# Performance work log

Hardware: AMD Instinct MI355X
Metric: run time of the kernel (lower is better)

Reference implementation:

```python
import jax, jax.numpy as jnp
import numpy as np

NUM_HEADS = 16
EMBED = 1024
HEAD = EMBED // NUM_HEADS  # 64
MAX_DIST = 4
NEG_INF = -1e30


def setup_inputs() -> dict:
    key = jax.random.key(0)
    ks = jax.random.split(key, 8)
    B, S = 2, 2048
    x = jax.random.normal(ks[0], (B, S, EMBED), dtype=jnp.float32)
    return {
        "k": x,  # self-attention: k == v == q values
        "v": x,
        "q": x,
        "Wk": jax.random.normal(ks[1], (EMBED, EMBED), dtype=jnp.float32) * 0.02,
        "Wv": jax.random.normal(ks[2], (EMBED, EMBED), dtype=jnp.float32) * 0.02,
        "Wq": jax.random.normal(ks[3], (EMBED, EMBED), dtype=jnp.float32) * 0.02,
        "Wo": jax.random.normal(ks[4], (EMBED, EMBED), dtype=jnp.float32) * 0.02,
        "p_params": jax.random.normal(ks[5], (HEAD, 2 * MAX_DIST + 1), dtype=jnp.float32) * 0.02,
    }


def reference(k, v, q, Wk, Wv, Wq, Wo, p_params):
    B, Kl, _ = k.shape
    Ql = q.shape[1]
    # torch nn.Linear(bias=False): y = x @ W.T
    kh = (k @ Wk.T).reshape(B, Kl, NUM_HEADS, HEAD).transpose(0, 2, 1, 3)
    vh = (v @ Wv.T).reshape(B, Kl, NUM_HEADS, HEAD).transpose(0, 2, 1, 3)
    qh = (q @ Wq.T).reshape(B, Ql, NUM_HEADS, HEAD).transpose(0, 2, 1, 3)
    qh = qh / jnp.sqrt(jnp.float32(HEAD))
    # content scores: [B,H,Q,K]
    scores0 = jnp.einsum("bhqd,bhkd->bhqk", qh, kh)
    # relative-position bias: q . p_params[:, r] for each bucket r, then gather per (i,j)
    bias = jnp.einsum("bhqd,dr->bhqr", qh, p_params)  # [B,H,Q,2M+1]
    d = jnp.clip(jnp.arange(Ql)[:, None] - jnp.arange(Kl)[None, :], -MAX_DIST, MAX_DIST) + MAX_DIST  # [Q,K]
    rel = bias[:, :, jnp.arange(Ql)[:, None], d]  # [B,H,Q,K]
    scores = scores0 + rel
    # causal mask
    causal = jnp.arange(Ql)[:, None] >= jnp.arange(Kl)[None, :]
    scores = jnp.where(causal[None, None], scores, NEG_INF)
    attn = jax.nn.softmax(scores, axis=-1)
    out = jnp.einsum("bhqk,bhkd->bhqd", attn, vh)
    out = out.transpose(0, 2, 1, 3).reshape(B, Ql, EMBED)
    return out @ Wo.T
```

## Files before the change

kernel.cpp:

```cpp
#include <hip/hip_runtime.h>


using short8  = __attribute__((ext_vector_type(8))) short;
using floatx4 = __attribute__((ext_vector_type(4))) float;
using float4v = __attribute__((ext_vector_type(4))) float;
using ushort4v = __attribute__((ext_vector_type(4))) unsigned short;
using uint2v  = __attribute__((ext_vector_type(2))) unsigned int;

#define LOG2E 1.4426950408889634f

__device__ __forceinline__ unsigned short f2bf(float f) {
  unsigned u = __float_as_uint(f);
  return (unsigned short)((u + 0x7FFFu + ((u >> 16) & 1u)) >> 16);
}
__device__ __forceinline__ float bf2f(unsigned short s) {
  return __uint_as_float(((unsigned)s) << 16);
}
__device__ __forceinline__ unsigned cvt_pk_bf16(float lo, float hi) {
  unsigned r;
  asm("v_cvt_pk_bf16_f32 %0, %1, %2" : "=v"(r) : "v"(lo), "v"(hi));
  return r;
}
__device__ __forceinline__ void gload_lds16(const void* g, void* l) {
  __builtin_amdgcn_global_load_lds(
      (const __attribute__((address_space(1))) unsigned int*)g,
      (__attribute__((address_space(3))) unsigned int*)l, 16, 0, 0);
}

__global__ void f2bf_kern(const float* __restrict__ in,
                          unsigned short* __restrict__ out, int n4) {
  int i = blockIdx.x * 256 + threadIdx.x;
  if (i >= n4) return;
  float4v v = ((const float4v*)in)[i];
  ushort4v o;
  o[0] = f2bf(v[0]); o[1] = f2bf(v[1]); o[2] = f2bf(v[2]); o[3] = f2bf(v[3]);
  ((ushort4v*)out)[i] = o;
}

__global__ void f2bfW_kern(const float* __restrict__ w0, unsigned short* o0,
                           const float* __restrict__ w1, unsigned short* o1,
                           const float* __restrict__ w2, unsigned short* o2,
                           const float* __restrict__ w3, unsigned short* o3) {
  int i = blockIdx.x * 256 + threadIdx.x;
  const float* in;
  unsigned short* out;
  switch (blockIdx.y) {
    case 0: in = w0; out = o0; break;
    case 1: in = w1; out = o1; break;
    case 2: in = w2; out = o2; break;
    default: in = w3; out = o3; break;
  }
  float4v v = ((const float4v*)in)[i];
  ushort4v o;
  o[0] = f2bf(v[0]); o[1] = f2bf(v[1]); o[2] = f2bf(v[2]); o[3] = f2bf(v[3]);
  ((ushort4v*)out)[i] = o;
}

__device__ __forceinline__ void gemm_core(
    const unsigned short* __restrict__ A, const unsigned short* __restrict__ B,
    void* __restrict__ Cv, int N, int K, int mBase, int nBase, float alpha,
    bool outbf, unsigned short* As, unsigned short* Bs) {
  const int tid = threadIdx.x;
  const int lane = tid & 63;
  const int w = tid >> 6;
  const int wr = w >> 1, wc = w & 1;
  const int lr = lane & 15, lg = lane >> 4;

  floatx4 acc[4][4] = {};

  for (int k0 = 0; k0 < K; k0 += 32) {
#pragma unroll
    for (int i = 0; i < 2; ++i) {
      int idx = i * 256 + tid;
      int row = idx >> 2, c8 = (idx & 3) * 8;
      gload_lds16(A + (size_t)(mBase + row) * K + (k0 + c8), As + idx * 8);
      gload_lds16(B + (size_t)(nBase + row) * K + (k0 + c8), Bs + idx * 8);
    }
    __syncthreads();
    short8 af[4], bfr[4];
#pragma unroll
    for (int mf = 0; mf < 4; ++mf)
      af[mf] = *(const short8*)(As + (wr * 64 + mf * 16 + lr) * 32 + lg * 8);
#pragma unroll
    for (int nf = 0; nf < 4; ++nf)
      bfr[nf] = *(const short8*)(Bs + (wc * 64 + nf * 16 + lr) * 32 + lg * 8);
#pragma unroll
    for (int mf = 0; mf < 4; ++mf)
#pragma unroll
      for (int nf = 0; nf < 4; ++nf)
        acc[mf][nf] = __builtin_amdgcn_mfma_f32_16x16x32_bf16(
            af[mf], bfr[nf], acc[mf][nf], 0, 0, 0);
    __syncthreads();
  }

#pragma unroll
  for (int mf = 0; mf < 4; ++mf)
#pragma unroll
    for (int nf = 0; nf < 4; ++nf)
#pragma unroll
      for (int r = 0; r < 4; ++r) {
        size_t row = (size_t)mBase + wr * 64 + mf * 16 + lg * 4 + r;
        size_t col = (size_t)nBase + wc * 64 + nf * 16 + lr;
        float v = acc[mf][nf][r] * alpha;
        if (outbf)
          ((unsigned short*)Cv)[row * (size_t)N + col] = f2bf(v);
        else
          ((float*)Cv)[row * (size_t)N + col] = v;
      }
}

__global__ __launch_bounds__(256, 2) void proj3_kern(
    const unsigned short* __restrict__ xbf, const unsigned short* __restrict__ wkb,
    unsigned short* __restrict__ khb,
    const unsigned short* __restrict__ wqb, unsigned short* __restrict__ qhb,
    const unsigned short* __restrict__ wvb, unsigned short* __restrict__ vtb) {
  __shared__ alignas(16) unsigned short As[128 * 32];
  __shared__ alignas(16) unsigned short Bs[128 * 32];
  int z = blockIdx.z;
  if (z == 0)
    gemm_core(xbf, wkb, khb, 1024, 1024, blockIdx.y * 128, blockIdx.x * 128,
              1.0f, true, As, Bs);
  else if (z == 1)
    gemm_core(xbf, wqb, qhb, 1024, 1024, blockIdx.y * 128, blockIdx.x * 128,
              0.125f, true, As, Bs);
  else
    gemm_core(wvb, xbf, vtb, 4096, 1024, blockIdx.x * 128, blockIdx.y * 128,
              1.0f, true, As, Bs);
}

__global__ __launch_bounds__(256, 2) void gemm_out_kern(
    const unsigned short* __restrict__ A, const unsigned short* __restrict__ B,
    float* __restrict__ C) {
  __shared__ alignas(16) unsigned short As[128 * 32];
  __shared__ alignas(16) unsigned short Bs[128 * 32];
  gemm_core(A, B, C, 1024, 1024, blockIdx.y * 128, blockIdx.x * 128, 1.0f,
            false, As, Bs);
}

__global__ __launch_bounds__(256, 3) void attn_kern(
    const unsigned short* __restrict__ qh,
    const unsigned short* __restrict__ kh,
    const unsigned short* __restrict__ vt,
    const float* __restrict__ pp,
    unsigned short* __restrict__ ao,
    unsigned short* __restrict__ opart,
    float* __restrict__ mbuf,
    float* __restrict__ lbuf) {
  __shared__ alignas(16) char smem[44032];
  unsigned short* Qs  = (unsigned short*)smem;
  unsigned short* Vs1 = (unsigned short*)(smem + 8192);
  unsigned short* Ks0 = (unsigned short*)(smem + 16384);
  unsigned short* Vs0 = (unsigned short*)(smem + 24576);
  unsigned short* Ps  = (unsigned short*)(smem + 32768);
  float* biasS = (float*)(smem + 40960);
  float* ppS   = (float*)(smem + 32768);

  const int tid = threadIdx.x;
  const int lane = tid & 63;
  const int w = tid >> 6;
  const int lr = lane & 15, lg = lane >> 4;
  const int hb = blockIdx.x;
  const int h = hb & 15, b = hb >> 4;
  const int u = blockIdx.y;

  int qt, k0, k1;
  if (u == 0)       { qt = 15;     k0 = 0;  k1 = 16; }
  else if (u <= 16) { qt = 15 + u; k0 = 0;  k1 = 16; }
  else if (u == 17) { qt = 31;     k0 = 16; k1 = 32; }
  else {
    int p = (u - 18) >> 1;
    if (((u - 18) & 1) == 0) { qt = 14 - p; k0 = 0;  k1 = qt + 1; }
    else                     { qt = 30 - p; k0 = 16; k1 = qt + 1; }
  }
  const bool partial = (qt >= 16);
  const int qbase = qt * 64;
  const size_t bsQ = (size_t)b * 2048 + qbase;

  const unsigned short* khB = kh + ((size_t)b * 2048) * 1024 + h * 64;
  const unsigned short* vtB = vt + ((size_t)h * 64) * 4096 + b * 2048;

  auto stage_kv = [&](int kbase, unsigned short* Kd, unsigned short* Vd) {
#pragma unroll
    for (int i = 0; i < 2; ++i) {
      int idx = i * 256 + tid;
      int row = idx >> 3, pc = idx & 7;
      int cl = pc ^ (row & 7);
      gload_lds16(khB + ((size_t)(kbase + row) << 10) + cl * 8, Kd + idx * 8);
      gload_lds16(vtB + ((size_t)row << 12) + kbase + cl * 8, Vd + idx * 8);
    }
  };

#pragma unroll
  for (int i = 0; i < 2; ++i) {
    int idx = i * 256 + tid;
    int row = idx >> 3, c8 = (idx & 7) * 8;
    gload_lds16(qh + (bsQ + row) * 1024 + h * 64 + c8, Qs + idx * 8);
  }
  for (int idx = tid; idx < 576; idx += 256) {
    int r = idx >> 6, d = idx & 63;
    ppS[r * 64 + d] = pp[d * 9 + r];
  }
  stage_kv(k0 * 64, Ks0, Vs0);
  __syncthreads();

  const int qrowL = w * 16 + lr;
  short8 aq[2];
#pragma unroll
  for (int c = 0; c < 2; ++c)
    aq[c] = *(const short8*)(Qs + qrowL * 64 + c * 32 + lg * 8);

  for (int idx = tid; idx < 576; idx += 256) {
    int row = idx / 9, r = idx - row * 9;
    const unsigned short* qrow = Qs + row * 64;
    const float* pr = ppS + r * 64;
    float s = 0.f;
#pragma unroll
    for (int d8 = 0; d8 < 8; ++d8) {
      short8 qv = *(const short8*)(qrow + d8 * 8);
#pragma unroll
      for (int j = 0; j < 8; ++j)
        s += bf2f((unsigned short)qv[j]) * pr[d8 * 8 + j];
    }
    biasS[row * 12 + r] = s;
  }
  __syncthreads();

  const int q_glob = qbase + w * 16 + lr;
  const float b8 = biasS[qrowL * 12 + 8];
  unsigned short* Pw = Ps + w * 1024;

  float m_run = -1e30f, l_run = 0.f;
  floatx4 o[4] = {};

  for (int kt = k0; kt < k1; ++kt) {
    const int kbase = kt * 64;
    const int cur = (kt - k0) & 1;
    unsigned short* Kc = cur ? Qs : Ks0;
    unsigned short* Vc = cur ? Vs1 : Vs0;
    if (kt + 1 < k1)
      stage_kv(kbase + 64, cur ? Ks0 : Qs, cur ? Vs0 : Vs1);

    floatx4 sa[4] = {};
    __builtin_amdgcn_s_setprio(1);
#pragma unroll
    for (int kf = 0; kf < 4; ++kf)
#pragma unroll
      for (int c = 0; c < 2; ++c) {
        int row = kf * 16 + lr;
        short8 ak = *(const short8*)(Kc + row * 64 +
                                     (((c * 4 + lg) ^ (lr & 7)) * 8));
        sa[kf] = __builtin_amdgcn_mfma_f32_16x16x32_bf16(ak, aq[c], sa[kf],
                                                         0, 0, 0);
      }
    __builtin_amdgcn_s_setprio(0);

    float bext;
    if (qbase + w * 16 >= kbase + 67) {
      bext = b8;
    } else {
      bext = 0.f;
#pragma unroll
      for (int kf = 0; kf < 4; ++kf)
#pragma unroll
        for (int r = 0; r < 4; ++r) {
          int dq = q_glob - (kbase + kf * 16 + lg * 4 + r);
          if (dq < 0)
            sa[kf][r] = -1e30f;
          else
            sa[kf][r] += biasS[qrowL * 12 + (dq > 4 ? 8 : dq + 4)];
        }
    }

    float mx = -1e30f;
#pragma unroll
    for (int kf = 0; kf < 4; ++kf)
#pragma unroll
      for (int r = 0; r < 4; ++r) mx = fmaxf(mx, sa[kf][r]);
    mx += bext;
    mx = fmaxf(mx, __shfl_xor(mx, 16, 64));
    mx = fmaxf(mx, __shfl_xor(mx, 32, 64));
    if (__any(mx > m_run + 8.f)) {
      float mn = fmaxf(m_run, mx);
      float al = __builtin_amdgcn_exp2f((m_run - mn) * LOG2E);
      m_run = mn;
      l_run *= al;
      float alo[4];
#pragma unroll
      for (int r = 0; r < 4; ++r) alo[r] = __shfl(al, lg * 4 + r, 64);
#pragma unroll
      for (int df = 0; df < 4; ++df)
#pragma unroll
        for (int r = 0; r < 4; ++r) o[df][r] *= alo[r];
    }

    const float c1 = (bext - m_run) * LOG2E;
    float rs = 0.f;
#pragma unroll
    for (int kf = 0; kf < 4; ++kf) {
      float p0 = __builtin_amdgcn_exp2f(fmaf(sa[kf][0], LOG2E, c1));
      float p1 = __builtin_amdgcn_exp2f(fmaf(sa[kf][1], LOG2E, c1));
      float p2 = __builtin_amdgcn_exp2f(fmaf(sa[kf][2], LOG2E, c1));
      float p3 = __builtin_amdgcn_exp2f(fmaf(sa[kf][3], LOG2E, c1));
      rs += (p0 + p1) + (p2 + p3);
      uint2v pk;
      pk[0] = cvt_pk_bf16(p0, p1);
      pk[1] = cvt_pk_bf16(p2, p3);
      int phys = (kf * 2 + (lg >> 1)) ^ (lr & 7);
      *(uint2v*)(Pw + lr * 64 + phys * 8 + (lg & 1) * 4) = pk;
    }
    rs += __shfl_xor(rs, 16, 64);
    rs += __shfl_xor(rs, 32, 64);
    l_run += rs;

    __builtin_amdgcn_s_setprio(1);
#pragma unroll
    for (int c = 0; c < 2; ++c) {
      short8 pa = *(const short8*)(Pw + lr * 64 +
                                   (((c * 4 + lg) ^ (lr & 7)) * 8));
#pragma unroll
      for (int df = 0; df < 4; ++df) {
        int row = df * 16 + lr;
        short8 bv = *(const short8*)(Vc + row * 64 +
                                     (((c * 4 + lg) ^ (lr & 7)) * 8));
        o[df] = __builtin_amdgcn_mfma_f32_16x16x32_bf16(pa, bv, o[df],
                                                        0, 0, 0);
      }
    }
    __builtin_amdgcn_s_setprio(0);
    __syncthreads();
  }

  if (!partial) {
    float rl[4];
#pragma unroll
    for (int r = 0; r < 4; ++r)
      rl[r] = __builtin_amdgcn_rcpf(__shfl(l_run, lg * 4 + r, 64));
    const size_t outRow0 = bsQ + w * 16 + lg * 4;
#pragma unroll
    for (int df = 0; df < 4; ++df)
#pragma unroll
      for (int r = 0; r < 4; ++r)
        ao[(outRow0 + r) * 1024 + h * 64 + df * 16 + lr] =
            f2bf(o[df][r] * rl[r]);
  } else {
    const int pid = (hb * 16 + (qt - 16)) * 2 + (k0 == 16 ? 1 : 0);
    unsigned short* op = opart + (size_t)pid * 4096;
#pragma unroll
    for (int df = 0; df < 4; ++df)
#pragma unroll
      for (int r = 0; r < 4; ++r)
        op[(w * 16 + lg * 4 + r) * 64 + df * 16 + lr] = f2bf(o[df][r]);
    if (lg == 0) {
      mbuf[pid * 64 + w * 16 + lr] = m_run;
      lbuf[pid * 64 + w * 16 + lr] = l_run;
    }
  }
}

__global__ void combine_kern(const unsigned short* __restrict__ opart,
                             const float* __restrict__ mbuf,
                             const float* __restrict__ lbuf,
                             unsigned short* __restrict__ ao) {
  const int t = blockIdx.x;
  const int hb = t >> 4;
  const int qtl = t & 15;
  const int qt = 16 + qtl;
  const int b = hb >> 4, h = hb & 15;
  const int pid0 = (hb * 16 + qtl) * 2, pid1 = pid0 + 1;
  const int row = threadIdx.x >> 2;
  const int colg = (threadIdx.x & 3) * 16;

  float m1 = mbuf[pid0 * 64 + row], m2 = mbuf[pid1 * 64 + row];
  float l1 = lbuf[pid0 * 64 + row], l2 = lbuf[pid1 * 64 + row];
  float m = fmaxf(m1, m2);
  float s1 = __builtin_amdgcn_exp2f((m1 - m) * LOG2E);
  float s2 = __builtin_amdgcn_exp2f((m2 - m) * LOG2E);
  float linv = 1.f / fmaf(l1, s1, l2 * s2);
  s1 *= linv; s2 *= linv;

  const unsigned short* O1 = opart + (size_t)pid0 * 4096 + row * 64 + colg;
  const unsigned short* O2 = opart + (size_t)pid1 * 4096 + row * 64 + colg;
  unsigned short* dst =
      ao + ((size_t)b * 2048 + qt * 64 + row) * 1024 + h * 64 + colg;
#pragma unroll
  for (int i = 0; i < 2; ++i) {
    short8 a = *(const short8*)(O1 + i * 8);
    short8 c = *(const short8*)(O2 + i * 8);
    short8 ov;
#pragma unroll
    for (int j = 0; j < 8; ++j)
      ov[j] = (short)f2bf(fmaf(bf2f((unsigned short)a[j]), s1,
                               bf2f((unsigned short)c[j]) * s2));
    *(short8*)(dst + i * 8) = ov;
  }
}

extern "C" void kernel_launch(void* const* d_in, const int* in_sizes, int n_in,
                              void* d_out, int out_size, void* d_ws,
                              size_t ws_size, hipStream_t stream) {
  const float* k_in = (const float*)d_in[0];
  const float* Wk = (const float*)d_in[3];
  const float* Wv = (const float*)d_in[4];
  const float* Wq = (const float*)d_in[5];
  const float* Wo = (const float*)d_in[6];
  const float* pp = (const float*)d_in[7];

  const size_t NX = 4096u * 1024u;
  const size_t NW = 1024u * 1024u;
  unsigned short* ws = (unsigned short*)d_ws;
  unsigned short* xbf = ws;
  unsigned short* wkb = xbf + NX;
  unsigned short* wvb = wkb + NW;
  unsigned short* wqb = wvb + NW;
  unsigned short* wob = wqb + NW;
  unsigned short* khb = wob + NW;
  unsigned short* vtb = khb + NX;
  unsigned short* qhb = vtb + NX;
  unsigned short* aob = qhb + NX;
  unsigned short* opart = aob + NX;
  float* mbuf = (float*)(opart + NX);
  float* lbuf = mbuf + 1024 * 64;

  (void)in_sizes; (void)n_in; (void)out_size; (void)ws_size;

  f2bf_kern<<<dim3(4096), dim3(256), 0, stream>>>(k_in, xbf, (int)(NX / 4));
  f2bfW_kern<<<dim3(1024, 4), dim3(256), 0, stream>>>(
      Wk, wkb, Wv, wvb, Wq, wqb, Wo, wob);

  proj3_kern<<<dim3(8, 32, 3), dim3(256), 0, stream>>>(
      xbf, wkb, khb, wqb, qhb, wvb, vtb);

  attn_kern<<<dim3(32, 48), dim3(256), 0, stream>>>(qhb, khb, vtb, pp, aob,
                                                    opart, mbuf, lbuf);
  combine_kern<<<dim3(512), dim3(256), 0, stream>>>(opart, mbuf, lbuf, aob);

  gemm_out_kern<<<dim3(8, 32), dim3(256), 0, stream>>>(aob, wob, (float*)d_out);
}
```

Measured before the change: 123.6 us.

## Redistribute softmax P via cross-lane shuffles instead of LDS round-trip

The per-wave P tile staging buffer in shared memory is removed. The bf16-packed probabilities are instead moved into the MFMA A-operand layout with ds_bpermute shuffles and lane selects. The smaller LDS footprint lets the launch bound rise from 3 to 4 blocks per CU, and ppS is relocated to overlap the Vs1 buffer. The cost is 16 shuffles per iteration and higher register pressure under the tighter occupancy bound.

```diff
diff --git a/kernel.cpp b/kernel.cpp
--- a/kernel.cpp
+++ b/kernel.cpp
@@ -5,7 +5,7 @@
 using floatx4 = __attribute__((ext_vector_type(4))) float;
 using float4v = __attribute__((ext_vector_type(4))) float;
 using ushort4v = __attribute__((ext_vector_type(4))) unsigned short;
-using uint2v  = __attribute__((ext_vector_type(2))) unsigned int;
+using uint4v  = __attribute__((ext_vector_type(4))) unsigned int;
 
 #define LOG2E 1.4426950408889634f
 
@@ -137,7 +137,7 @@
             false, As, Bs);
 }
 
-__global__ __launch_bounds__(256, 3) void attn_kern(
+__global__ __launch_bounds__(256, 4) void attn_kern(
     const unsigned short* __restrict__ qh,
     const unsigned short* __restrict__ kh,
     const unsigned short* __restrict__ vt,
@@ -146,14 +146,13 @@
     unsigned short* __restrict__ opart,
     float* __restrict__ mbuf,
     float* __restrict__ lbuf) {
-  __shared__ alignas(16) char smem[44032];
+  __shared__ alignas(16) char smem[35840];
   unsigned short* Qs  = (unsigned short*)smem;
   unsigned short* Vs1 = (unsigned short*)(smem + 8192);
   unsigned short* Ks0 = (unsigned short*)(smem + 16384);
   unsigned short* Vs0 = (unsigned short*)(smem + 24576);
-  unsigned short* Ps  = (unsigned short*)(smem + 32768);
-  float* biasS = (float*)(smem + 40960);
-  float* ppS   = (float*)(smem + 32768);
+  float* biasS = (float*)(smem + 32768);
+  float* ppS   = (float*)(smem + 8192);
 
   const int tid = threadIdx.x;
   const int lane = tid & 63;
@@ -227,7 +226,8 @@
 
   const int q_glob = qbase + w * 16 + lr;
   const float b8 = biasS[qrowL * 12 + 8];
-  unsigned short* Pw = Ps + w * 1024;
+  const int sl0 = lr + 16 * ((lg & 1) * 2);
+  const int sl1 = sl0 + 16;
 
   float m_run = -1e30f, l_run = 0.f;
   floatx4 o[4] = {};
@@ -295,6 +295,7 @@
 
     const float c1 = (bext - m_run) * LOG2E;
     float rs = 0.f;
+    unsigned pk[4][2];
 #pragma unroll
     for (int kf = 0; kf < 4; ++kf) {
       float p0 = __builtin_amdgcn_exp2f(fmaf(sa[kf][0], LOG2E, c1));
@@ -302,30 +303,43 @@
       float p2 = __builtin_amdgcn_exp2f(fmaf(sa[kf][2], LOG2E, c1));
       float p3 = __builtin_amdgcn_exp2f(fmaf(sa[kf][3], LOG2E, c1));
       rs += (p0 + p1) + (p2 + p3);
-      uint2v pk;
-      pk[0] = cvt_pk_bf16(p0, p1);
-      pk[1] = cvt_pk_bf16(p2, p3);
-      int phys = (kf * 2 + (lg >> 1)) ^ (lr & 7);
-      *(uint2v*)(Pw + lr * 64 + phys * 8 + (lg & 1) * 4) = pk;
+      pk[kf][0] = cvt_pk_bf16(p0, p1);
+      pk[kf][1] = cvt_pk_bf16(p2, p3);
     }
     rs += __shfl_xor(rs, 16, 64);
     rs += __shfl_xor(rs, 32, 64);
     l_run += rs;
 
+    short8 pa[2];
+#pragma unroll
+    for (int c = 0; c < 2; ++c) {
+      unsigned a0 = __shfl((int)pk[2 * c][0], sl0, 64);
+      unsigned b0 = __shfl((int)pk[2 * c + 1][0], sl0, 64);
+      unsigned a1 = __shfl((int)pk[2 * c][1], sl0, 64);
+      unsigned b1 = __shfl((int)pk[2 * c + 1][1], sl0, 64);
+      unsigned a2 = __shfl((int)pk[2 * c][0], sl1, 64);
+      unsigned b2 = __shfl((int)pk[2 * c + 1][0], sl1, 64);
+      unsigned a3 = __shfl((int)pk[2 * c][1], sl1, 64);
+      unsigned b3 = __shfl((int)pk[2 * c + 1][1], sl1, 64);
+      uint4v t;
+      t[0] = (lg & 2) ? b0 : a0;
+      t[1] = (lg & 2) ? b1 : a1;
+      t[2] = (lg & 2) ? b2 : a2;
+      t[3] = (lg & 2) ? b3 : a3;
+      pa[c] = *(short8*)&t;
+    }
+
     __builtin_amdgcn_s_setprio(1);
 #pragma unroll
-    for (int c = 0; c < 2; ++c) {
-      short8 pa = *(const short8*)(Pw + lr * 64 +
-                                   (((c * 4 + lg) ^ (lr & 7)) * 8));
+    for (int c = 0; c < 2; ++c)
 #pragma unroll
       for (int df = 0; df < 4; ++df) {
         int row = df * 16 + lr;
         short8 bv = *(const short8*)(Vc + row * 64 +
                                      (((c * 4 + lg) ^ (lr & 7)) * 8));
-        o[df] = __builtin_amdgcn_mfma_f32_16x16x32_bf16(pa, bv, o[df],
+        o[df] = __builtin_amdgcn_mfma_f32_16x16x32_bf16(pa[c], bv, o[df],
                                                         0, 0, 0);
       }
-    }
     __builtin_amdgcn_s_setprio(0);
     __syncthreads();
   }
```

After: 131.0 us. 6.0% more time.
